# Performance work log

Measured on AMD Instinct MI355X. Metric: run time of the kernel, lower is better.

The kernel has to match this reference:

```python
import jax, jax.numpy as jnp
import numpy as np

EPS = 1e-5
SLOPE = 0.01  # nn.LeakyReLU default
K = 32
SIGMA = 1.0

def lrelu(x):
    return jnp.where(x >= 0, x, SLOPE * x)

def bn(x, gamma, beta, axes):
    # BatchNorm in training mode (fresh module, batch statistics)
    mu = jnp.mean(x, axis=axes, keepdims=True)
    var = jnp.var(x, axis=axes, keepdims=True)
    return (x - mu) * jax.lax.rsqrt(var + EPS) * gamma + beta

def knn_gather(x, k):
    # x: (B, N, C) -> neighbor features (B, N, k, C) by smallest squared distance
    sq = jnp.sum(x * x, axis=-1)
    d = sq[:, :, None] - 2.0 * jnp.einsum('bnc,bmc->bnm', x, x) + sq[:, None, :]
    idx = jax.lax.top_k(-d, k)[1]                      # (B, N, k)
    nbr = jax.vmap(lambda xb, ib: xb[ib])(x, idx)      # (B, N, k, C)
    return nbr

def edge_conv(x, w1, g1, b1, w2, g2, b2):
    # DGCNN EdgeConv: feat = [x_j - x_i, x_i] -> 1x1 conv/BN/LeakyReLU x2 -> max over k
    nbr = knn_gather(x, K)                             # (B, N, k, C)
    xc = x[:, :, None, :]
    feat = jnp.concatenate([nbr - xc, jnp.broadcast_to(xc, nbr.shape)], axis=-1)
    h = lrelu(bn(jnp.einsum('bnkc,oc->bnko', feat, w1), g1, b1, (0, 1, 2)))
    h = lrelu(bn(jnp.einsum('bnkc,oc->bnko', h, w2), g2, b2, (0, 1, 2)))
    return jnp.max(h, axis=2)                          # (B, N, C_out)

def gaussian_kernel_conv(xnei, centers):
    # xnei: (B, N, k, C), centers: (O, C) -> (B, N, O)
    d = (jnp.sum(xnei * xnei, -1)[..., None]
         - 2.0 * jnp.einsum('bnkc,oc->bnko', xnei, centers)
         + jnp.sum(centers * centers, -1))
    return jnp.sum(jnp.exp(-d / (2.0 * SIGMA ** 2)), axis=2)

def setup_inputs() -> dict:
    key = jax.random.key(0)
    ks = jax.random.split(key, 16)
    s = 0.05
    return {
        'x': jax.random.normal(ks[0], (2, 3, 64, 64), jnp.float32),
        'kc_centers': jax.random.normal(ks[1], (128, 3), jnp.float32),
        'e1_w1': jax.random.normal(ks[2], (64, 6), jnp.float32) * s,
        'e1_g1': jnp.ones((64,), jnp.float32), 'e1_b1': jnp.zeros((64,), jnp.float32),
        'e1_w2': jax.random.normal(ks[3], (64, 64), jnp.float32) * s,
        'e1_g2': jnp.ones((64,), jnp.float32), 'e1_b2': jnp.zeros((64,), jnp.float32),
        'e2_w1': jax.random.normal(ks[4], (128, 128), jnp.float32) * s,
        'e2_g1': jnp.ones((128,), jnp.float32), 'e2_b1': jnp.zeros((128,), jnp.float32),
        'e2_w2': jax.random.normal(ks[5], (128, 128), jnp.float32) * s,
        'e2_g2': jnp.ones((128,), jnp.float32), 'e2_b2': jnp.zeros((128,), jnp.float32),
        'w1': jax.random.normal(ks[6], (1024, 256), jnp.float32) * s,
        'g1': jnp.ones((1024,), jnp.float32), 'b1': jnp.zeros((1024,), jnp.float32),
        'w2': jax.random.normal(ks[7], (512, 1024), jnp.float32) * s,
        'g2': jnp.ones((512,), jnp.float32), 'b2': jnp.zeros((512,), jnp.float32),
        'w3': jax.random.normal(ks[8], (256, 512), jnp.float32) * s,
        'g3': jnp.ones((256,), jnp.float32), 'b3': jnp.zeros((256,), jnp.float32),
        'w4': jax.random.normal(ks[9], (9, 256), jnp.float32) * s,
    }

def reference(x, kc_centers, e1_w1, e1_g1, e1_b1, e1_w2, e1_g2, e1_b2,
              e2_w1, e2_g1, e2_b1, e2_w2, e2_g2, e2_b2,
              w1, g1, b1, w2, g2, b2, w3, g3, b3, w4):
    bs, f, c, n = x.shape
    # knn over the (B, c*n, 3) point cloud
    pts = x.reshape(bs, -1, c * n).transpose(0, 2, 1)
    xnei = knn_gather(pts, K)                               # (B, c*n, K, 3)
    kernels = gaussian_kernel_conv(xnei, kc_centers)        # (B, c*n, 128)
    # EdgeConv chain on reshape-view (matches torch reshape semantics exactly)
    xe = x.reshape(bs, c * n, -1)                           # (B, c*n, 3)
    xe = edge_conv(xe, e1_w1, e1_g1, e1_b1, e1_w2, e1_g2, e1_b2)   # (B, c*n, 64)
    xe = edge_conv(xe, e2_w1, e2_g1, e2_b1, e2_w2, e2_g2, e2_b2)   # (B, c*n, 128)
    h = jnp.concatenate([xe.reshape(bs, -1, c, n),
                         kernels.transpose(0, 2, 1).reshape(bs, -1, c, n)], axis=1)  # (B,256,c,n)
    def cbr(h, w, g, b):
        h = jnp.einsum('bchw,oc->bohw', h, w)               # 1x1 conv, no bias
        return lrelu(bn(h, g[None, :, None, None], b[None, :, None, None], (0, 2, 3)))
    h = cbr(h, w1, g1, b1)
    h = cbr(h, w2, g2, b2)
    h = cbr(h, w3, g3, b3)
    h = jnp.einsum('bchw,oc->bohw', h, w4)                  # (B, 9, c, n)
    h = jnp.max(jnp.max(h, axis=3), axis=2)                 # (B, 9)
    out = h + jnp.eye(3, dtype=h.dtype).reshape(1, 9)
    return out.reshape(bs, 3, 3)
```

## Files before the change

### kernel.cpp

```cpp
#include <hip/hip_runtime.h>
#include <hip/hip_fp16.h>
#include <math.h>

#define WN 4096
#define NP 8192
#define KK 32
#define EPSB 1e-5f

typedef __attribute__((ext_vector_type(8))) short s8v;
typedef __attribute__((ext_vector_type(4))) short s4v;
typedef __attribute__((ext_vector_type(4))) float f4v;

__device__ __forceinline__ float lrelu(float x){ return fmaxf(x, 0.01f*x); }
__device__ __forceinline__ float rlane(float v, int c){
  return __int_as_float(__builtin_amdgcn_readlane(__float_as_int(v), c));
}
__device__ __forceinline__ short f2bf(float f){
  unsigned u = __float_as_uint(f);
  u = (u + 0x7fffu + ((u>>16)&1u)) >> 16;
  return (short)u;
}
__device__ __forceinline__ float bf2f(short s){
  return __uint_as_float(((unsigned)(unsigned short)s) << 16);
}

__global__ void k_prep(const float* __restrict__ x, float* __restrict__ pts, float* __restrict__ xe0,
                       float* __restrict__ sqp, float* __restrict__ sqe,
                       float4* __restrict__ pts4, float4* __restrict__ xe04){
  int i = blockIdx.x*256 + threadIdx.x;
  if(i >= NP) return;
  int b = i>>12, p = i&4095;
  const float* xb = x + b*12288;
  float a0 = xb[p], a1 = xb[4096+p], a2 = xb[8192+p];
  pts[i*3+0]=a0; pts[i*3+1]=a1; pts[i*3+2]=a2;
  float sp = (a0*a0 + a1*a1) + a2*a2;
  sqp[i] = sp;
  pts4[i] = make_float4(a0,a1,a2,sp);
  float e0 = xb[p*3+0], e1 = xb[p*3+1], e2 = xb[p*3+2];
  xe0[i*3+0]=e0; xe0[i*3+1]=e1; xe0[i*3+2]=e2;
  float se = (e0*e0 + e1*e1) + e2*e2;
  sqe[i] = se;
  xe04[i] = make_float4(e0,e1,e2,se);
}

__device__ __forceinline__ void bitonic64(float& d, int& m, int l){
  #pragma unroll
  for(int k=2;k<=64;k<<=1){
    #pragma unroll
    for(int j=k>>1;j>0;j>>=1){
      float pd = __shfl_xor(d, j);
      int pm = __shfl_xor(m, j);
      bool pLess = (pd < d);
      bool dirUp = ((l & k) == 0);
      bool lower = ((l & j) == 0);
      bool take = dirUp ? (lower ? pLess : !pLess) : (lower ? !pLess : pLess);
      if(take){ d = pd; m = pm; }
    }
  }
}

__device__ __forceinline__ void kmerge(const float2* __restrict__ buf, int cnt, int l,
                                       float& lv, int& li){
  __builtin_amdgcn_wave_barrier();
  float md; int mi;
  if(l < 32){ md = lv; mi = li; }
  else{
    int i = l - 32;
    if(i < cnt){ float2 e = buf[i]; md = e.x; mi = __float_as_int(e.y); }
    else{ md = 3.4e38f; mi = 0x7fffffff; }
  }
  bitonic64(md, mi, l);
  if(l < 32){ lv = md; li = mi; }
}

__device__ __forceinline__ void topk_buf(float d, int m, int l, float2* __restrict__ buf,
                                         int& cnt, float& thr, float& lv, int& li){
  bool alive = d < thr;
  unsigned long long mask = __ballot(alive);
  while(mask){
    int nsurv = __popcll(mask);
    int space = 32 - cnt;
    int prefix = __popcll(mask & ((1ull<<l)-1ull));
    bool store = alive && (prefix < space);
    if(store) buf[cnt + prefix] = make_float2(d, __int_as_float(m));
    cnt += (nsurv < space) ? nsurv : space;
    alive = alive && !store;
    if(cnt == 32){
      kmerge(buf, 32, l, lv, li);
      cnt = 0;
      thr = rlane(lv, 31);
      alive = alive && (d < thr);
    }
    mask = __ballot(alive);
  }
}

__global__ __launch_bounds__(256) void k_knn3(const float4* __restrict__ pnt4, int* __restrict__ idx){
  __shared__ float2 bufs[4][32];
  int l = threadIdx.x&63;
  int wid = threadIdx.x>>6;
  int q = blockIdx.x*4 + wid;
  int b = q>>12, qr = q&4095;
  const float4* pb = pnt4 + ((size_t)b<<12);
  float2* buf = bufs[wid];
  float4 qv = pb[qr];
  float q0=qv.x, q1=qv.y, q2=qv.z, sqq=qv.w;
  float4 nc = pb[l + 64];
  float dd; int mm = l;
  {
    float4 c = pb[l];
    float dot = q0*c.x + q1*c.y + q2*c.z;
    dd = (sqq - 2.0f*dot) + c.w;
  }
  bitonic64(dd, mm, l);
  float lv = (l<32) ? dd : 3.4e38f;
  int li = (l<32) ? mm : 0x7fffffff;
  float thr = rlane(lv, 31);
  int cnt = 0;
  #pragma unroll 4
  for(int j=1;j<64;j++){
    float4 c = nc;
    nc = pb[l + (((j+1)&63)<<6)];
    float dot = q0*c.x + q1*c.y + q2*c.z;
    float d = (sqq - 2.0f*dot) + c.w;
    topk_buf(d, l + (j<<6), l, buf, cnt, thr, lv, li);
  }
  if(cnt) kmerge(buf, cnt, l, lv, li);
  if(l < 32) idx[(size_t)q*KK + l] = li;
}

__global__ __launch_bounds__(256) void k_knn_sel(const __half2* __restrict__ D, int* __restrict__ idx){
  __shared__ float2 bufs[4][32];
  int l = threadIdx.x&63;
  int wid = threadIdx.x>>6;
  int q = blockIdx.x*4 + wid;
  int b = q>>12, qr = q&4095;
  const __half2* row = D + ((size_t)b<<23) + ((size_t)qr<<11);
  float2* buf = bufs[wid];
  __half2 h0 = row[l];
  __half2 nh = row[l + 64];
  float2 f0 = __half22float2(h0);
  float dmin, dmax; int mmin, mmax;
  if(f0.x <= f0.y){ dmin=f0.x; mmin=2*l;   dmax=f0.y; mmax=2*l+1; }
  else            { dmin=f0.y; mmin=2*l+1; dmax=f0.x; mmax=2*l;   }
  bitonic64(dmin, mmin, l);
  float lv = (l<32) ? dmin : 3.4e38f;
  int li = (l<32) ? mmin : 0x7fffffff;
  float thr = rlane(lv, 31);
  int cnt = 0;
  topk_buf(dmax, mmax, l, buf, cnt, thr, lv, li);
  #pragma unroll 4
  for(int j=1;j<32;j++){
    __half2 h = nh;
    nh = row[l + (((j+1)&31)<<6)];
    float2 g = __half22float2(h);
    int base = 2*(l + (j<<6));
    topk_buf(g.x, base,   l, buf, cnt, thr, lv, li);
    topk_buf(g.y, base+1, l, buf, cnt, thr, lv, li);
  }
  if(cnt) kmerge(buf, cnt, l, lv, li);
  if(l < 32) idx[(size_t)q*KK + l] = li;
}

__global__ __launch_bounds__(128) void k_gauss(const float* __restrict__ pts, const float* __restrict__ sqp,
                                               const int* __restrict__ idxP, const float* __restrict__ cen,
                                               float* __restrict__ kout){
  __shared__ float nbx[KK], nby[KK], nbz[KK], nsq[KK];
  int p = blockIdx.x; int b = p>>12; int t = threadIdx.x;
  if(t < KK){
    int id = idxP[(size_t)p*KK + t] + (b<<12);
    nbx[t]=pts[id*3]; nby[t]=pts[id*3+1]; nbz[t]=pts[id*3+2];
    nsq[t]=sqp[id];
  }
  __syncthreads();
  float c0=cen[t*3], c1=cen[t*3+1], c2=cen[t*3+2];
  float sqc=(c0*c0+c1*c1)+c2*c2;
  float acc=0.f;
  #pragma unroll
  for(int k=0;k<KK;k++){
    float dot = nbx[k]*c0 + nby[k]*c1 + nbz[k]*c2;
    float d = (nsq[k] - 2.0f*dot) + sqc;
    acc += __expf(-0.5f*d);
  }
  kout[(size_t)((b<<7)+t)*4096 + (p&4095)] = acc;
}

__global__ void k_fin(const float* __restrict__ psum, const float* __restrict__ psq, int NW, int C, float Nn,
                      const float* __restrict__ g, const float* __restrict__ be,
                      float* __restrict__ sc, float* __restrict__ sh){
  int o = blockIdx.x, t = threadIdx.x;
  float s=0.f, q=0.f;
  for(int w=t; w<NW; w+=256){ s += psum[(size_t)w*C+o]; q += psq[(size_t)w*C+o]; }
  __shared__ float ls[256], lq[256];
  ls[t]=s; lq[t]=q; __syncthreads();
  for(int st=128; st; st>>=1){ if(t<st){ ls[t]+=ls[t+st]; lq[t]+=lq[t+st]; } __syncthreads(); }
  if(t==0){
    float mu = ls[0]/Nn;
    float var = lq[0]/Nn - mu*mu; if(var<0.f) var=0.f;
    float s1 = g[o]*rsqrtf(var + EPSB);
    sc[o]=s1; sh[o]=be[o]-mu*s1;
  }
}

__global__ __launch_bounds__(256) void k_ec1mom(const float* __restrict__ xe0, const int* __restrict__ idx1,
                                                float* __restrict__ pmom){
  int tid = blockIdx.x*256 + threadIdx.x;
  int l = threadIdx.x & 63;
  int wid = tid >> 6;
  float a[27];
  #pragma unroll
  for(int v=0;v<27;v++) a[v]=0.f;
  #pragma unroll
  for(int u=0;u<2;u++){
    int s = tid*2 + u;
    int p = s>>5;
    int bb = (p>>12)<<12;
    int id = bb + idx1[s];
    const float* nb = xe0 + (size_t)id*3;
    const float* xc = xe0 + (size_t)p*3;
    float f[6];
    f[0]=nb[0]-xc[0]; f[1]=nb[1]-xc[1]; f[2]=nb[2]-xc[2];
    f[3]=xc[0]; f[4]=xc[1]; f[5]=xc[2];
    int v=0;
    #pragma unroll
    for(int i=0;i<6;i++){
      #pragma unroll
      for(int j=i;j<6;j++){ a[v] = fmaf(f[i], f[j], a[v]); v++; }
    }
    #pragma unroll
    for(int i=0;i<6;i++) a[21+i] += f[i];
  }
  #pragma unroll
  for(int v=0;v<27;v++){
    float t = a[v];
    #pragma unroll
    for(int off=32; off; off>>=1) t += __shfl_xor(t, off);
    if(l==0) pmom[v*2048 + wid] = t;
  }
}

__global__ void k_msum(const float* __restrict__ pmom, float* __restrict__ mom){
  int v = blockIdx.x; int t = threadIdx.x;
  float s=0.f;
  for(int i=t;i<2048;i+=256) s += pmom[v*2048+i];
  __shared__ float ls[256];
  ls[t]=s; __syncthreads();
  for(int st=128; st; st>>=1){ if(t<st) ls[t]+=ls[t+st]; __syncthreads(); }
  if(t==0) mom[v]=ls[0];
}

__global__ void k_ec1bn(const float* __restrict__ mom, const float* __restrict__ w1,
                        const float* __restrict__ g, const float* __restrict__ be,
                        float* __restrict__ sc, float* __restrict__ sh){
  __shared__ float M[27];
  int t = threadIdx.x;
  if(t<27) M[t]=mom[t];
  __syncthreads();
  if(t<64){
    float w[6];
    #pragma unroll
    for(int c=0;c<6;c++) w[c]=w1[t*6+c];
    float qf=0.f, m1=0.f;
    int v=0;
    #pragma unroll
    for(int i=0;i<6;i++){
      #pragma unroll
      for(int j=i;j<6;j++){ qf += (i==j?1.f:2.f)*w[i]*w[j]*M[v]; v++; }
    }
    #pragma unroll
    for(int i=0;i<6;i++) m1 += w[i]*M[21+i];
    float N = 262144.f;
    float mu = m1/N;
    float var = qf/N - mu*mu; if(var<0.f) var=0.f;
    float s1 = g[t]*rsqrtf(var + EPSB);
    sc[t]=s1; sh[t]=be[t]-mu*s1;
  }
}

__global__ __launch_bounds__(256) void k_ec1g2m(const float* __restrict__ xe0, const int* __restrict__ idx1,
                                                const short* __restrict__ w2b, const float* __restrict__ w1,
                                                const float* __restrict__ s1, const float* __restrict__ t1,
                                                float* __restrict__ h2m, float* __restrict__ psum,
                                                float* __restrict__ psq){
  __shared__ short sA[8192], sB[8192];
  __shared__ float feat[6][128];
  __shared__ float w1l[384];
  __shared__ float bnS[64], bnT[64];
  __shared__ float srs[4][64], srq[4][64];
  int t = threadIdx.x;
  int blk = blockIdx.x;
  int s0 = blk*128;
  int pbase = s0>>5;
  int bb = (s0>>17)<<12;
  #pragma unroll
  for(int i=0;i<4;i++){
    int slot = t + i*256;
    *(s8v*)&sA[slot*8] = *(const s8v*)&w2b[slot*8];
  }
  for(int i=t; i<384; i+=256) w1l[i] = w1[i];
  if(t<64){ bnS[t]=s1[t]; bnT[t]=t1[t]; }
  if(t < 128){
    int s = s0 + t;
    int p = pbase + (t>>5);
    int id = bb + idx1[s];
    const float* nb = xe0 + (size_t)id*3;
    const float* xc = xe0 + (size_t)p*3;
    float x0 = xc[0], x1 = xc[1], x2 = xc[2];
    feat[0][t] = nb[0]-x0; feat[1][t] = nb[1]-x1; feat[2][t] = nb[2]-x2;
    feat[3][t] = x0; feat[4][t] = x1; feat[5][t] = x2;
  }
  __syncthreads();
  #pragma unroll
  for(int i=0;i<4;i++){
    int e = t + (i<<8);
    int n = e & 127;
    int kb8 = e >> 7;
    int k0 = kb8*8;
    float f0=feat[0][n], f1=feat[1][n], f2=feat[2][n];
    float f3=feat[3][n], f4=feat[4][n], f5=feat[5][n];
    s8v r;
    #pragma unroll
    for(int j=0;j<8;j++){
      int k = k0 + j;
      float h = w1l[k*6+0]*f0 + w1l[k*6+1]*f1 + w1l[k*6+2]*f2
              + w1l[k*6+3]*f3 + w1l[k*6+4]*f4 + w1l[k*6+5]*f5;
      r[j] = f2bf(lrelu(fmaf(h, bnS[k], bnT[k])));
    }
    int chunk = (k0>>5)*8 + (n>>4);
    int lane_ = ((k0>>3)&3)*16 + (n&15);
    *(s8v*)&sB[chunk*512 + lane_*8] = r;
  }
  __syncthreads();
  int lane = t&63, w = t>>6;
  f4v acc[4][2];
  #pragma unroll
  for(int i=0;i<4;i++){
    #pragma unroll
    for(int j=0;j<2;j++) acc[i][j] = (f4v)(0.f);
  }
  #pragma unroll
  for(int kh=0;kh<2;kh++){
    s8v av[4], bv[2];
    #pragma unroll
    for(int f=0;f<4;f++) av[f] = *(const s8v*)&sA[(kh*8 + f)*512 + lane*8];
    #pragma unroll
    for(int g=0;g<2;g++) bv[g] = *(const s8v*)&sB[(kh*8 + w*2 + g)*512 + lane*8];
    #pragma unroll
    for(int fm=0;fm<4;fm++){
      #pragma unroll
      for(int fn=0;fn<2;fn++)
        acc[fm][fn] = __builtin_amdgcn_mfma_f32_16x16x32_bf16(av[fm], bv[fn], acc[fm][fn], 0, 0, 0);
    }
  }
  int l15 = lane&15, l4 = (lane>>4)*4;
  int point = pbase + w;
  #pragma unroll
  for(int fm=0;fm<4;fm++){
    #pragma unroll
    for(int r=0;r<4;r++){
      int m = fm*16 + l4 + r;
      float a0 = acc[fm][0][r], a1 = acc[fm][1][r];
      float sr = a0 + a1;
      float sq = a0*a0 + a1*a1;
      float mx = fmaxf(a0, a1);
      #pragma unroll
      for(int off=1; off<16; off<<=1){
        sr += __shfl_xor(sr, off);
        sq += __shfl_xor(sq, off);
        mx = fmaxf(mx, __shfl_xor(mx, off));
      }
      if(l15==0){
        srs[w][m] = sr; srq[w][m] = sq;
        h2m[(size_t)point*64 + m] = mx;
      }
    }
  }
  __syncthreads();
  if(t<64){
    psum[(size_t)blk*64+t] = (srs[0][t]+srs[1][t]) + (srs[2][t]+srs[3][t]);
    psq[(size_t)blk*64+t]  = (srq[0][t]+srq[1][t]) + (srq[2][t]+srq[3][t]);
  }
}

__global__ __launch_bounds__(256) void k_ec1fin(const float* __restrict__ h2m, const float* __restrict__ s2,
                                                const float* __restrict__ t2, float* __restrict__ xe1,
                                                float* __restrict__ xe1T, float* __restrict__ sqx){
  int gid = blockIdx.x*256 + threadIdx.x;
  int p = gid>>6, l = gid&63;
  float v = lrelu(fmaf(h2m[(size_t)p*64+l], s2[l], t2[l]));
  xe1[(size_t)p*64+l] = v;
  int b=p>>12, pr=p&4095;
  xe1T[(size_t)(b*64+l)*4096 + pr] = v;
  float sq = v*v;
  #pragma unroll
  for(int off=32; off; off>>=1) sq += __shfl_xor(sq, off);
  if(l==0) sqx[p]=sq;
}

__global__ __launch_bounds__(256) void k_dgemm_m(const short* __restrict__ X, const float* __restrict__ sqx,
                                                 __half* __restrict__ D){
  __shared__ short sA[8192], sB[8192];
  int t = threadIdx.x;
  int lane = t&63, w = t>>6;
  int wm4 = (w>>1)*4, wn4 = (w&1)*4;
  int mb = blockIdx.y, nb = blockIdx.x, b = blockIdx.z;
  const short* AG = X + (size_t)(b*32 + mb)*8192;
  const short* BG = X + (size_t)(b*32 + nb)*8192;
  #pragma unroll
  for(int i=0;i<4;i++){
    int slot = t + i*256;
    *(s8v*)&sA[slot*8] = *(const s8v*)&AG[slot*8];
    *(s8v*)&sB[slot*8] = *(const s8v*)&BG[slot*8];
  }
  __syncthreads();
  f4v acc[4][4];
  #pragma unroll
  for(int i=0;i<4;i++){
    #pragma unroll
    for(int j=0;j<4;j++) acc[i][j] = (f4v)(0.f);
  }
  #pragma unroll
  for(int kh=0;kh<2;kh++){
    s8v av[4], bv[4];
    #pragma unroll
    for(int f=0;f<4;f++) av[f] = *(const s8v*)&sA[(kh*8 + wm4 + f)*512 + lane*8];
    #pragma unroll
    for(int f=0;f<4;f++) bv[f] = *(const s8v*)&sB[(kh*8 + wn4 + f)*512 + lane*8];
    #pragma unroll
    for(int fm=0;fm<4;fm++){
      #pragma unroll
      for(int fn=0;fn<4;fn++)
        acc[fm][fn] = __builtin_amdgcn_mfma_f32_16x16x32_bf16(av[fm], bv[fn], acc[fm][fn], 0, 0, 0);
    }
  }
  const float* sb = sqx + (b<<12);
  __half* Db = D + ((size_t)b<<24);
  int l15 = lane&15, l4 = (lane>>4)*4;
  #pragma unroll
  for(int fm=0;fm<4;fm++){
    int m0 = mb*128 + wm4*16 + fm*16 + l4;
    float sm0 = sb[m0], sm1 = sb[m0+1], sm2 = sb[m0+2], sm3 = sb[m0+3];
    #pragma unroll
    for(int fn=0;fn<4;fn++){
      int n = nb*128 + wn4*16 + fn*16 + l15;
      float sqn = sb[n];
      __half2 h01 = __floats2half2_rn((sm0 + sqn) - 2.f*acc[fm][fn][0],
                                      (sm1 + sqn) - 2.f*acc[fm][fn][1]);
      __half2 h23 = __floats2half2_rn((sm2 + sqn) - 2.f*acc[fm][fn][2],
                                      (sm3 + sqn) - 2.f*acc[fm][fn][3]);
      __half2* p = (__half2*)&Db[(size_t)n*4096 + m0];
      p[0] = h01; p[1] = h23;
    }
  }
}

__global__ __launch_bounds__(256) void k_ec2m1(const float* __restrict__ xe1, const int* __restrict__ idx2,
                                               const short* __restrict__ wb, short* __restrict__ h1,
                                               float* __restrict__ psum, float* __restrict__ psq){
  __shared__ short sA[8192], sB[8192];
  __shared__ float cts[4][64];
  __shared__ int nid[128];
  __shared__ float srs[2][128], srq[2][128];
  int t = threadIdx.x;
  int blk = blockIdx.x;
  int s0 = blk*128;
  int pbase = s0>>5;
  int bb = (s0>>17)<<12;
  if(t<128) nid[t] = (idx2[s0+t] + bb)<<6;
  cts[t>>6][t&63] = xe1[(size_t)(pbase + (t>>6))*64 + (t&63)];
  int lane = t&63, w = t>>6;
  int wm4 = (w>>1)*4, wn4 = (w&1)*4;
  f4v acc[4][4];
  #pragma unroll
  for(int i=0;i<4;i++){
    #pragma unroll
    for(int j=0;j<4;j++) acc[i][j] = (f4v)(0.f);
  }
  for(int st=0; st<2; ++st){
    __syncthreads();
    #pragma unroll
    for(int i=0;i<4;i++){
      int slot = t + i*256;
      *(s8v*)&sA[slot*8] = *(const s8v*)&wb[st*8192 + slot*8];
      int chunk = slot>>6, li = slot&63;
      int n = (chunk&7)*16 + (li&15);
      int c = ((chunk>>3)<<5) + ((li>>4)<<3);
      float v[8];
      if(st==0){
        const float* src = xe1 + nid[n] + c;
        float4 a0 = *(const float4*)src;
        float4 a1 = *(const float4*)(src+4);
        const float* cc = &cts[n>>5][c];
        float4 c0 = *(const float4*)cc;
        float4 c1 = *(const float4*)(cc+4);
        v[0]=a0.x-c0.x; v[1]=a0.y-c0.y; v[2]=a0.z-c0.z; v[3]=a0.w-c0.w;
        v[4]=a1.x-c1.x; v[5]=a1.y-c1.y; v[6]=a1.z-c1.z; v[7]=a1.w-c1.w;
      } else {
        const float* cc = &cts[n>>5][c];
        float4 c0 = *(const float4*)cc;
        float4 c1 = *(const float4*)(cc+4);
        v[0]=c0.x; v[1]=c0.y; v[2]=c0.z; v[3]=c0.w;
        v[4]=c1.x; v[5]=c1.y; v[6]=c1.z; v[7]=c1.w;
      }
      s8v r;
      #pragma unroll
      for(int j=0;j<8;j++) r[j] = f2bf(v[j]);
      *(s8v*)&sB[slot*8] = r;
    }
    __syncthreads();
    #pragma unroll
    for(int kh=0;kh<2;kh++){
      s8v av[4], bv[4];
      #pragma unroll
      for(int f=0;f<4;f++) av[f] = *(const s8v*)&sA[(kh*8 + wm4 + f)*512 + lane*8];
      #pragma unroll
      for(int f=0;f<4;f++) bv[f] = *(const s8v*)&sB[(kh*8 + wn4 + f)*512 + lane*8];
      #pragma unroll
      for(int fm=0;fm<4;fm++){
        #pragma unroll
        for(int fn=0;fn<4;fn++)
          acc[fm][fn] = __builtin_amdgcn_mfma_f32_16x16x32_bf16(av[fm], bv[fn], acc[fm][fn], 0, 0, 0);
      }
    }
  }
  int l15 = lane&15, l4 = (lane>>4)<<2;
  #pragma unroll
  for(int fm=0;fm<4;fm++){
    int mb_ = wm4*16 + fm*16 + l4;
    #pragma unroll
    for(int fn=0;fn<4;fn++){
      int n = wn4*16 + fn*16 + l15;
      s4v hw;
      hw[0]=f2bf(acc[fm][fn][0]); hw[1]=f2bf(acc[fm][fn][1]);
      hw[2]=f2bf(acc[fm][fn][2]); hw[3]=f2bf(acc[fm][fn][3]);
      *(s4v*)&h1[(size_t)(s0+n)*128 + mb_] = hw;
    }
    #pragma unroll
    for(int r=0;r<4;r++){
      float sr = (acc[fm][0][r]+acc[fm][1][r]) + (acc[fm][2][r]+acc[fm][3][r]);
      float sq = (acc[fm][0][r]*acc[fm][0][r]+acc[fm][1][r]*acc[fm][1][r])
               + (acc[fm][2][r]*acc[fm][2][r]+acc[fm][3][r]*acc[fm][3][r]);
      #pragma unroll
      for(int off=1; off<16; off<<=1){ sr += __shfl_xor(sr, off); sq += __shfl_xor(sq, off); }
      if(l15==0){ srs[w&1][mb_+r] = sr; srq[w&1][mb_+r] = sq; }
    }
  }
  __syncthreads();
  if(t<128){
    psum[(size_t)blk*128+t] = srs[0][t]+srs[1][t];
    psq[(size_t)blk*128+t]  = srq[0][t]+srq[1][t];
  }
}

__global__ __launch_bounds__(256) void k_ec2m2(const short* __restrict__ h1, const short* __restrict__ wb,
                                               const float* __restrict__ s1, const float* __restrict__ t1,
                                               float* __restrict__ h2max, float* __restrict__ psum,
                                               float* __restrict__ psq){
  __shared__ short sA[8192], sB[8192];
  __shared__ float bnS[128], bnT[128];
  __shared__ float srs[2][128], srq[2][128];
  int t = threadIdx.x;
  int blk = blockIdx.x;
  int s0 = blk*128;
  int pbase = s0>>5;
  if(t<128){ bnS[t]=s1[t]; bnT[t]=t1[t]; }
  int lane = t&63, w = t>>6;
  int wm4 = (w>>1)*4, wn4 = (w&1)*4;
  f4v acc[4][4];
  #pragma unroll
  for(int i=0;i<4;i++){
    #pragma unroll
    for(int j=0;j<4;j++) acc[i][j] = (f4v)(0.f);
  }
  for(int st=0; st<2; ++st){
    __syncthreads();
    #pragma unroll
    for(int i=0;i<4;i++){
      int slot = t + i*256;
      *(s8v*)&sA[slot*8] = *(const s8v*)&wb[st*8192 + slot*8];
      int chunk = slot>>6, li = slot&63;
      int n = (chunk&7)*16 + (li&15);
      int c = st*64 + ((chunk>>3)<<5) + ((li>>4)<<3);
      s8v hv = *(const s8v*)&h1[(size_t)(s0+n)*128 + c];
      s8v r;
      #pragma unroll
      for(int j=0;j<8;j++){
        float v = bf2f(hv[j]);
        r[j] = f2bf(lrelu(fmaf(v, bnS[c+j], bnT[c+j])));
      }
      *(s8v*)&sB[slot*8] = r;
    }
    __syncthreads();
    #pragma unroll
    for(int kh=0;kh<2;kh++){
      s8v av[4], bv[4];
      #pragma unroll
      for(int f=0;f<4;f++) av[f] = *(const s8v*)&sA[(kh*8 + wm4 + f)*512 + lane*8];
      #pragma unroll
      for(int f=0;f<4;f++) bv[f] = *(const s8v*)&sB[(kh*8 + wn4 + f)*512 + lane*8];
      #pragma unroll
      for(int fm=0;fm<4;fm++){
        #pragma unroll
        for(int fn=0;fn<4;fn++)
          acc[fm][fn] = __builtin_amdgcn_mfma_f32_16x16x32_bf16(av[fm], bv[fn], acc[fm][fn], 0, 0, 0);
      }
    }
  }
  int l15 = lane&15, l4 = (lane>>4)<<2;
  int pp0 = wn4>>1;
  #pragma unroll
  for(int fm=0;fm<4;fm++){
    int mb_ = wm4*16 + fm*16 + l4;
    #pragma unroll
    for(int r=0;r<4;r++){
      float sr = (acc[fm][0][r]+acc[fm][1][r]) + (acc[fm][2][r]+acc[fm][3][r]);
      float sq = (acc[fm][0][r]*acc[fm][0][r]+acc[fm][1][r]*acc[fm][1][r])
               + (acc[fm][2][r]*acc[fm][2][r]+acc[fm][3][r]*acc[fm][3][r]);
      float m0 = fmaxf(acc[fm][0][r], acc[fm][1][r]);
      float m1 = fmaxf(acc[fm][2][r], acc[fm][3][r]);
      #pragma unroll
      for(int off=1; off<16; off<<=1){ sr += __shfl_xor(sr, off); sq += __shfl_xor(sq, off); }
      #pragma unroll
      for(int off=1; off<16; off<<=1){ m0 = fmaxf(m0, __shfl_xor(m0, off)); m1 = fmaxf(m1, __shfl_xor(m1, off)); }
      if(l15==0){
        srs[w&1][mb_+r] = sr; srq[w&1][mb_+r] = sq;
        h2max[(size_t)(pbase+pp0)*128   + mb_+r] = m0;
        h2max[(size_t)(pbase+pp0+1)*128 + mb_+r] = m1;
      }
    }
  }
  __syncthreads();
  if(t<128){
    psum[(size_t)blk*128+t] = srs[0][t]+srs[1][t];
    psq[(size_t)blk*128+t]  = srq[0][t]+srq[1][t];
  }
}

__global__ void k_xe2fin(float* __restrict__ xe2, const float* __restrict__ s2, const float* __restrict__ t2){
  int i = blockIdx.x*256 + threadIdx.x;
  if(i >= NP*128) return;
  int o = i&127;
  xe2[i] = lrelu(fmaf(xe2[i], s2[o], t2[o]));
}

__global__ void k_transpose(const float* __restrict__ w, float* __restrict__ wT, int O, int C){
  int i = blockIdx.x*256 + threadIdx.x;
  if(i >= O*C) return;
  int o = i / C, c = i % C;
  wT[(size_t)c*O + o] = w[i];
}

__global__ void k_wprep(const float* __restrict__ w, short* __restrict__ wb, int M, int K){
  int tid = blockIdx.x*256 + threadIdx.x;
  int m = tid % M, kb8 = tid / M;
  int k0 = kb8*8;
  float4 v0 = *(const float4*)&w[(size_t)m*K + k0];
  float4 v1 = *(const float4*)&w[(size_t)m*K + k0 + 4];
  s8v r;
  r[0]=f2bf(v0.x); r[1]=f2bf(v0.y); r[2]=f2bf(v0.z); r[3]=f2bf(v0.w);
  r[4]=f2bf(v1.x); r[5]=f2bf(v1.y); r[6]=f2bf(v1.z); r[7]=f2bf(v1.w);
  int region = (m>>7)*(K>>6) + (k0>>6);
  int chunk = ((kb8>>2)&1)*8 + ((m>>4)&7);
  int lane = (kb8&3)*16 + (m&15);
  *(s8v*)&wb[(size_t)region*8192 + chunk*512 + lane*8] = r;
}

__global__ void k_bprep(const float* __restrict__ in, const float* __restrict__ sc, const float* __restrict__ sh,
                        short* __restrict__ ob, int K){
  int tid = blockIdx.x*256 + threadIdx.x;
  int n = tid & 8191, kb8 = tid >> 13;
  int k0 = kb8*8;
  int b = n>>12, s = n&4095;
  const float* ib = in + ((size_t)b*K + k0)*4096 + s;
  float v[8];
  #pragma unroll
  for(int j=0;j<8;j++) v[j] = ib[(size_t)j*4096];
  if(sc){
    #pragma unroll
    for(int j=0;j<8;j++) v[j] = lrelu(fmaf(v[j], sc[k0+j], sh[k0+j]));
  }
  s8v r;
  #pragma unroll
  for(int j=0;j<8;j++) r[j] = f2bf(v[j]);
  int region = (n>>7)*(K>>6) + (k0>>6);
  int chunk = ((kb8>>2)&1)*8 + ((n>>4)&7);
  int lane = (kb8&3)*16 + (n&15);
  *(s8v*)&ob[(size_t)region*8192 + chunk*512 + lane*8] = r;
}

__global__ void k_bprep1(const float* __restrict__ xe2, const float* __restrict__ kr,
                         short* __restrict__ ob){
  int tid = blockIdx.x*256 + threadIdx.x;
  int n = tid & 8191, kb8 = tid >> 13;
  int k0 = kb8*8;
  int b = n>>12, s = n&4095;
  const float* ib;
  if(k0 < 128) ib = xe2 + (size_t)b*524288 + (size_t)k0*4096 + s;
  else         ib = kr + ((size_t)(b*128 + (k0-128)))*4096 + s;
  float v[8];
  #pragma unroll
  for(int j=0;j<8;j++) v[j] = ib[(size_t)j*4096];
  s8v r;
  #pragma unroll
  for(int j=0;j<8;j++) r[j] = f2bf(v[j]);
  int region = (n>>7)*4 + (k0>>6);
  int chunk = ((kb8>>2)&1)*8 + ((n>>4)&7);
  int lane = (kb8&3)*16 + (n&15);
  *(s8v*)&ob[(size_t)region*8192 + chunk*512 + lane*8] = r;
}

__global__ __launch_bounds__(256) void k_gmm(const short* __restrict__ A, const short* __restrict__ B,
                                             float* __restrict__ out, int M, int K){
  __shared__ short sA[8192], sB[8192];
  int t = threadIdx.x;
  int lane = t&63;
  int w = t>>6;
  int wm4 = (w>>1)*4, wn4 = (w&1)*4;
  int mb = blockIdx.y, nb = blockIdx.x;
  int ksteps = K>>6;
  const short* AG = A + (size_t)mb*ksteps*8192;
  const short* BG = B + (size_t)nb*ksteps*8192;
  f4v acc[4][4];
  #pragma unroll
  for(int i=0;i<4;i++){
    #pragma unroll
    for(int j=0;j<4;j++) acc[i][j] = (f4v)(0.f);
  }
  for(int st=0; st<ksteps; ++st){
    __syncthreads();
    #pragma unroll
    for(int i=0;i<4;i++){
      int slot = t + i*256;
      *(s8v*)&sA[slot*8] = *(const s8v*)&AG[(size_t)st*8192 + slot*8];
      *(s8v*)&sB[slot*8] = *(const s8v*)&BG[(size_t)st*8192 + slot*8];
    }
    __syncthreads();
    #pragma unroll
    for(int kh=0;kh<2;kh++){
      s8v av[4], bv[4];
      #pragma unroll
      for(int f=0;f<4;f++) av[f] = *(const s8v*)&sA[(kh*8 + wm4 + f)*512 + lane*8];
      #pragma unroll
      for(int f=0;f<4;f++) bv[f] = *(const s8v*)&sB[(kh*8 + wn4 + f)*512 + lane*8];
      #pragma unroll
      for(int fm=0;fm<4;fm++){
        #pragma unroll
        for(int fn=0;fn<4;fn++)
          acc[fm][fn] = __builtin_amdgcn_mfma_f32_16x16x32_bf16(av[fm], bv[fn], acc[fm][fn], 0, 0, 0);
      }
    }
  }
  int l15 = lane&15, l4 = (lane>>4)*4;
  #pragma unroll
  for(int fm=0;fm<4;fm++){
    int mrow = mb*128 + wm4*16 + fm*16 + l4;
    #pragma unroll
    for(int fn=0;fn<4;fn++){
      int n = nb*128 + wn4*16 + fn*16 + l15;
      int b = n>>12, s = n&4095;
      float* ob = out + ((size_t)b*M + mrow)*4096 + s;
      #pragma unroll
      for(int r=0;r<4;r++) ob[(size_t)r*4096] = acc[fm][fn][r];
    }
  }
}

__global__ void k_cstats(const float* __restrict__ buf, int C, const float* __restrict__ g,
                         const float* __restrict__ be, float* __restrict__ sc, float* __restrict__ sh){
  int o = blockIdx.x, t = threadIdx.x;
  float s=0.f, q=0.f;
  for(int i=t;i<8192;i+=256){
    int b=i>>12, ss_=i&4095;
    float v = buf[(size_t)(b*C+o)*4096 + ss_];
    s+=v; q+=v*v;
  }
  __shared__ float ls[256], lq[256];
  ls[t]=s; lq[t]=q; __syncthreads();
  for(int st=128; st; st>>=1){ if(t<st){ ls[t]+=ls[t+st]; lq[t]+=lq[t+st]; } __syncthreads(); }
  if(t==0){
    float mu = ls[0]/8192.f;
    float var = lq[0]/8192.f - mu*mu; if(var<0.f) var=0.f;
    float s1 = g[o]*rsqrtf(var + EPSB);
    sc[o]=s1; sh[o]=be[o]-mu*s1;
  }
}

__global__ __launch_bounds__(256) void k_final4(const float* __restrict__ c3, const float* __restrict__ w4T,
                                                const float* __restrict__ sc, const float* __restrict__ sh,
                                                float* __restrict__ pmax){
  int b = blockIdx.y, st = blockIdx.x;
  int t = threadIdx.x; int s = st*256 + t;
  float acc[9];
  #pragma unroll
  for(int j=0;j<9;j++) acc[j]=0.f;
  const float* ib = c3 + (size_t)b*256*4096;
  for(int c=0;c<256;c++){
    float x = lrelu(fmaf(ib[(size_t)c*4096+s], sc[c], sh[c]));
    #pragma unroll
    for(int j=0;j<9;j++) acc[j]=fmaf(x, w4T[c*9+j], acc[j]);
  }
  __shared__ float red[256];
  for(int j=0;j<9;j++){
    red[t]=acc[j]; __syncthreads();
    for(int stp=128; stp; stp>>=1){ if(t<stp) red[t]=fmaxf(red[t],red[t+stp]); __syncthreads(); }
    if(t==0) pmax[(b*16+st)*9 + j]=red[0];
    __syncthreads();
  }
}

__global__ void k_out(const float* __restrict__ pmax, float* __restrict__ out){
  int i = threadIdx.x;
  if(i<18){
    int b=i/9, o=i%9;
    float m=-3.4e38f;
    for(int k=0;k<16;k++) m=fmaxf(m, pmax[(b*16+k)*9+o]);
    out[i] = m + ((o==0||o==4||o==8)?1.f:0.f);
  }
}

extern "C" void kernel_launch(void* const* d_in, const int* in_sizes, int n_in,
                              void* d_out, int out_size, void* d_ws, size_t ws_size,
                              hipStream_t stream){
  const float* x    = (const float*)d_in[0];
  const float* kc   = (const float*)d_in[1];
  const float* e1w1 = (const float*)d_in[2];
  const float* e1g1 = (const float*)d_in[3];
  const float* e1b1 = (const float*)d_in[4];
  const float* e1w2 = (const float*)d_in[5];
  const float* e1g2 = (const float*)d_in[6];
  const float* e1b2 = (const float*)d_in[7];
  const float* e2w1 = (const float*)d_in[8];
  const float* e2g1 = (const float*)d_in[9];
  const float* e2b1 = (const float*)d_in[10];
  const float* e2w2 = (const float*)d_in[11];
  const float* e2g2 = (const float*)d_in[12];
  const float* e2b2 = (const float*)d_in[13];
  const float* w1   = (const float*)d_in[14];
  const float* g1   = (const float*)d_in[15];
  const float* b1   = (const float*)d_in[16];
  const float* w2   = (const float*)d_in[17];
  const float* g2   = (const float*)d_in[18];
  const float* b2   = (const float*)d_in[19];
  const float* w3   = (const float*)d_in[20];
  const float* g3   = (const float*)d_in[21];
  const float* b3   = (const float*)d_in[22];
  const float* w4   = (const float*)d_in[23];

  if(ws_size < 156061696ull) return;
  char* ws = (char*)d_ws;
  float* pts   = (float*)(ws + 0);
  float* xe0   = (float*)(ws + 98304);
  float* sqp   = (float*)(ws + 196608);
  float* sqe   = (float*)(ws + 229376);
  float* sqx1  = (float*)(ws + 262144);
  float* xe1   = (float*)(ws + 294912);
  float* xe1T  = (float*)(ws + 2392064);
  float* xe2   = (float*)(ws + 4489216);
  float* kr    = (float*)(ws + 8683520);
  int*   idxP  = (int*)  (ws + 12877824);
  int*   idx1  = (int*)  (ws + 13926400);
  int*   idx2  = (int*)  (ws + 14974976);
  float* psum  = (float*)(ws + 16023552);
  float* psq   = (float*)(ws + 17072128);
  float* par   = (float*)(ws + 18120704);
  float* pmax  = (float*)(ws + 18153472);
  short* wb0   = (short*)(ws + 18157568);
  float* wT4   = (float*)(ws + 21827584);
  float* hbuf  = (float*)(ws + 21843968);
  short* wbe1  = (short*)(ws + 0);
  short* wbe2  = (short*)(ws + 65536);
  float4* pts4 = (float4*)(ws + 4489216);
  float4* xe04 = (float4*)(ws + 4489216 + 131072);
  short* actB  = (short*)(ws + 88952832);
  short* xpack = (short*)(ws + 88952832);
  short* h1b   = (short*)(ws + 21843968);
  short* wb1   = (short*)(ws + 105730048);
  short* wb2   = (short*)(ws + 106254336);
  short* wb3   = (short*)(ws + 107302912);
  float* pmom  = psum;
  float* momv  = psq;

  float* e1s1 = par+0;    float* e1t1 = par+64;
  float* e1s2 = par+128;  float* e1t2 = par+192;
  float* e2s1 = par+256;  float* e2t1 = par+384;
  float* e2s2 = par+512;  float* e2t2 = par+640;
  float* c1s  = par+768;  float* c1t  = par+1792;
  float* c2s  = par+2816; float* c2t  = par+3328;
  float* c3s  = par+3840; float* c3t  = par+4096;

  float* c1out = hbuf + 2097152;
  float* c2out = hbuf + 10485760;
  float* c3out = hbuf + 14680064;

  hipLaunchKernelGGL(k_prep, dim3(32), dim3(256), 0, stream, x, pts, xe0, sqp, sqe, pts4, xe04);
  hipLaunchKernelGGL(k_knn3, dim3(2048), dim3(256), 0, stream, pts4, idxP);
  hipLaunchKernelGGL(k_knn3, dim3(2048), dim3(256), 0, stream, xe04, idx1);
  hipLaunchKernelGGL(k_gauss, dim3(8192), dim3(128), 0, stream, pts, sqp, idxP, kc, kr);

  hipLaunchKernelGGL(k_wprep, dim3(2), dim3(256), 0, stream, e1w2, wb0, 64, 64);
  hipLaunchKernelGGL(k_ec1mom, dim3(512), dim3(256), 0, stream, xe0, idx1, pmom);
  hipLaunchKernelGGL(k_msum, dim3(27), dim3(256), 0, stream, pmom, momv);
  hipLaunchKernelGGL(k_ec1bn, dim3(1), dim3(64), 0, stream, momv, e1w1, e1g1, e1b1, e1s1, e1t1);
  hipLaunchKernelGGL(k_ec1g2m, dim3(2048), dim3(256), 0, stream, xe0, idx1, wb0, e1w1, e1s1, e1t1, hbuf, psum, psq);
  hipLaunchKernelGGL(k_fin, dim3(64), dim3(256), 0, stream, psum, psq, 2048, 64, 262144.f, e1g2, e1b2, e1s2, e1t2);
  hipLaunchKernelGGL(k_ec1fin, dim3(2048), dim3(256), 0, stream, hbuf, e1s2, e1t2, xe1, xe1T, sqx1);

  hipLaunchKernelGGL(k_wprep, dim3(256), dim3(256), 0, stream, xe1, xpack, 8192, 64);
  hipLaunchKernelGGL(k_dgemm_m, dim3(32,32,2), dim3(256), 0, stream, xpack, sqx1, (__half*)hbuf);
  hipLaunchKernelGGL(k_knn_sel, dim3(2048), dim3(256), 0, stream, (const __half2*)hbuf, idx2);

  hipLaunchKernelGGL(k_wprep, dim3(8), dim3(256), 0, stream, e2w1, wbe1, 128, 128);
  hipLaunchKernelGGL(k_wprep, dim3(8), dim3(256), 0, stream, e2w2, wbe2, 128, 128);
  hipLaunchKernelGGL(k_ec2m1, dim3(2048), dim3(256), 0, stream, xe1, idx2, wbe1, h1b, psum, psq);
  hipLaunchKernelGGL(k_fin, dim3(128), dim3(256), 0, stream, psum, psq, 2048, 128, 262144.f, e2g1, e2b1, e2s1, e2t1);
  hipLaunchKernelGGL(k_ec2m2, dim3(2048), dim3(256), 0, stream, h1b, wbe2, e2s1, e2t1, xe2, psum, psq);
  hipLaunchKernelGGL(k_fin, dim3(128), dim3(256), 0, stream, psum, psq, 2048, 128, 262144.f, e2g2, e2b2, e2s2, e2t2);
  hipLaunchKernelGGL(k_xe2fin, dim3(4096), dim3(256), 0, stream, xe2, e2s2, e2t2);

  hipLaunchKernelGGL(k_wprep, dim3(128), dim3(256), 0, stream, w1, wb1, 1024, 256);
  hipLaunchKernelGGL(k_wprep, dim3(256), dim3(256), 0, stream, w2, wb2, 512, 1024);
  hipLaunchKernelGGL(k_wprep, dim3(64),  dim3(256), 0, stream, w3, wb3, 256, 512);
  hipLaunchKernelGGL(k_transpose, dim3((9*256+255)/256), dim3(256), 0, stream, w4, wT4, 9, 256);

  hipLaunchKernelGGL(k_bprep1, dim3(1024), dim3(256), 0, stream, xe2, kr, actB);
  hipLaunchKernelGGL(k_gmm, dim3(64,8), dim3(256), 0, stream, wb1, actB, c1out, 1024, 256);
  hipLaunchKernelGGL(k_cstats, dim3(1024), dim3(256), 0, stream, c1out, 1024, g1, b1, c1s, c1t);

  hipLaunchKernelGGL(k_bprep, dim3(4096), dim3(256), 0, stream, c1out, c1s, c1t, actB, 1024);
  hipLaunchKernelGGL(k_gmm, dim3(64,4), dim3(256), 0, stream, wb2, actB, c2out, 512, 1024);
  hipLaunchKernelGGL(k_cstats, dim3(512), dim3(256), 0, stream, c2out, 512, g2, b2, c2s, c2t);

  hipLaunchKernelGGL(k_bprep, dim3(2048), dim3(256), 0, stream, c2out, c2s, c2t, actB, 512);
  hipLaunchKernelGGL(k_gmm, dim3(64,2), dim3(256), 0, stream, wb3, actB, c3out, 256, 512);
  hipLaunchKernelGGL(k_cstats, dim3(256), dim3(256), 0, stream, c3out, 256, g3, b3, c3s, c3t);

  hipLaunchKernelGGL(k_final4, dim3(16,2), dim3(256), 0, stream, c3out, wT4, c3s, c3t, pmax);
  hipLaunchKernelGGL(k_out, dim3(1), dim3(32), 0, stream, pmax, (float*)d_out);
}
```

Baseline: 517.2 us.

## Recompute first EdgeConv2 GEMM in fused kernel instead of storing h1 intermediate

```diff
diff --git a/kernel.cpp b/kernel.cpp
--- a/kernel.cpp
+++ b/kernel.cpp
@@ -454,9 +454,9 @@
   }
 }
 
-__global__ __launch_bounds__(256) void k_ec2m1(const float* __restrict__ xe1, const int* __restrict__ idx2,
-                                               const short* __restrict__ wb, short* __restrict__ h1,
-                                               float* __restrict__ psum, float* __restrict__ psq){
+__global__ __launch_bounds__(256) void k_ec2s(const float* __restrict__ xe1, const int* __restrict__ idx2,
+                                              const short* __restrict__ wb,
+                                              float* __restrict__ psum, float* __restrict__ psq){
   __shared__ short sA[8192], sB[8192];
   __shared__ float cts[4][64];
   __shared__ int nid[128];
@@ -528,14 +528,6 @@
   for(int fm=0;fm<4;fm++){
     int mb_ = wm4*16 + fm*16 + l4;
     #pragma unroll
-    for(int fn=0;fn<4;fn++){
-      int n = wn4*16 + fn*16 + l15;
-      s4v hw;
-      hw[0]=f2bf(acc[fm][fn][0]); hw[1]=f2bf(acc[fm][fn][1]);
-      hw[2]=f2bf(acc[fm][fn][2]); hw[3]=f2bf(acc[fm][fn][3]);
-      *(s4v*)&h1[(size_t)(s0+n)*128 + mb_] = hw;
-    }
-    #pragma unroll
     for(int r=0;r<4;r++){
       float sr = (acc[fm][0][r]+acc[fm][1][r]) + (acc[fm][2][r]+acc[fm][3][r]);
       float sq = (acc[fm][0][r]*acc[fm][0][r]+acc[fm][1][r]*acc[fm][1][r])
@@ -552,18 +544,24 @@
   }
 }
 
-__global__ __launch_bounds__(256) void k_ec2m2(const short* __restrict__ h1, const short* __restrict__ wb,
-                                               const float* __restrict__ s1, const float* __restrict__ t1,
-                                               float* __restrict__ h2max, float* __restrict__ psum,
-                                               float* __restrict__ psq){
+__global__ __launch_bounds__(256) void k_ec2f(const float* __restrict__ xe1, const int* __restrict__ idx2,
+                                              const short* __restrict__ wb1e, const short* __restrict__ wb2e,
+                                              const float* __restrict__ s1, const float* __restrict__ t1,
+                                              float* __restrict__ h2max, float* __restrict__ psum,
+                                              float* __restrict__ psq){
   __shared__ short sA[8192], sB[8192];
+  __shared__ short h1L[128*136];
+  __shared__ float cts[4][64];
+  __shared__ int nid[128];
   __shared__ float bnS[128], bnT[128];
   __shared__ float srs[2][128], srq[2][128];
   int t = threadIdx.x;
   int blk = blockIdx.x;
   int s0 = blk*128;
   int pbase = s0>>5;
-  if(t<128){ bnS[t]=s1[t]; bnT[t]=t1[t]; }
+  int bb = (s0>>17)<<12;
+  if(t<128){ nid[t] = (idx2[s0+t] + bb)<<6; bnS[t]=s1[t]; bnT[t]=t1[t]; }
+  cts[t>>6][t&63] = xe1[(size_t)(pbase + (t>>6))*64 + (t&63)];
   int lane = t&63, w = t>>6;
   int wm4 = (w>>1)*4, wn4 = (w&1)*4;
   f4v acc[4][4];
@@ -577,17 +575,30 @@
     #pragma unroll
     for(int i=0;i<4;i++){
       int slot = t + i*256;
-      *(s8v*)&sA[slot*8] = *(const s8v*)&wb[st*8192 + slot*8];
+      *(s8v*)&sA[slot*8] = *(const s8v*)&wb1e[st*8192 + slot*8];
       int chunk = slot>>6, li = slot&63;
       int n = (chunk&7)*16 + (li&15);
-      int c = st*64 + ((chunk>>3)<<5) + ((li>>4)<<3);
-      s8v hv = *(const s8v*)&h1[(size_t)(s0+n)*128 + c];
+      int c = ((chunk>>3)<<5) + ((li>>4)<<3);
+      float v[8];
+      if(st==0){
+        const float* src = xe1 + nid[n] + c;
+        float4 a0 = *(const float4*)src;
+        float4 a1 = *(const float4*)(src+4);
+        const float* cc = &cts[n>>5][c];
+        float4 c0 = *(const float4*)cc;
+        float4 c1 = *(const float4*)(cc+4);
+        v[0]=a0.x-c0.x; v[1]=a0.y-c0.y; v[2]=a0.z-c0.z; v[3]=a0.w-c0.w;
+        v[4]=a1.x-c1.x; v[5]=a1.y-c1.y; v[6]=a1.z-c1.z; v[7]=a1.w-c1.w;
+      } else {
+        const float* cc = &cts[n>>5][c];
+        float4 c0 = *(const float4*)cc;
+        float4 c1 = *(const float4*)(cc+4);
+        v[0]=c0.x; v[1]=c0.y; v[2]=c0.z; v[3]=c0.w;
+        v[4]=c1.x; v[5]=c1.y; v[6]=c1.z; v[7]=c1.w;
+      }
       s8v r;
       #pragma unroll
-      for(int j=0;j<8;j++){
-        float v = bf2f(hv[j]);
-        r[j] = f2bf(lrelu(fmaf(v, bnS[c+j], bnT[c+j])));
-      }
+      for(int j=0;j<8;j++) r[j] = f2bf(v[j]);
       *(s8v*)&sB[slot*8] = r;
     }
     __syncthreads();
@@ -607,17 +618,66 @@
     }
   }
   int l15 = lane&15, l4 = (lane>>4)<<2;
-  int pp0 = wn4>>1;
   #pragma unroll
   for(int fm=0;fm<4;fm++){
     int mb_ = wm4*16 + fm*16 + l4;
+    float b0 = bnS[mb_], b1 = bnS[mb_+1], b2 = bnS[mb_+2], b3 = bnS[mb_+3];
+    float c0 = bnT[mb_], c1 = bnT[mb_+1], c2 = bnT[mb_+2], c3 = bnT[mb_+3];
+    #pragma unroll
+    for(int fn=0;fn<4;fn++){
+      int n = wn4*16 + fn*16 + l15;
+      s4v hw;
+      hw[0]=f2bf(lrelu(fmaf(acc[fm][fn][0], b0, c0)));
+      hw[1]=f2bf(lrelu(fmaf(acc[fm][fn][1], b1, c1)));
+      hw[2]=f2bf(lrelu(fmaf(acc[fm][fn][2], b2, c2)));
+      hw[3]=f2bf(lrelu(fmaf(acc[fm][fn][3], b3, c3)));
+      *(s4v*)&h1L[n*136 + mb_] = hw;
+    }
+  }
+  f4v acc2[4][4];
+  #pragma unroll
+  for(int i=0;i<4;i++){
+    #pragma unroll
+    for(int j=0;j<4;j++) acc2[i][j] = (f4v)(0.f);
+  }
+  for(int st=0; st<2; ++st){
+    __syncthreads();
+    #pragma unroll
+    for(int i=0;i<4;i++){
+      int slot = t + i*256;
+      *(s8v*)&sA[slot*8] = *(const s8v*)&wb2e[st*8192 + slot*8];
+      int chunk = slot>>6, li = slot&63;
+      int n = (chunk&7)*16 + (li&15);
+      int c = st*64 + ((chunk>>3)<<5) + ((li>>4)<<3);
+      *(s8v*)&sB[slot*8] = *(const s8v*)&h1L[n*136 + c];
+    }
+    __syncthreads();
+    #pragma unroll
+    for(int kh=0;kh<2;kh++){
+      s8v av[4], bv[4];
+      #pragma unroll
+      for(int f=0;f<4;f++) av[f] = *(const s8v*)&sA[(kh*8 + wm4 + f)*512 + lane*8];
+      #pragma unroll
+      for(int f=0;f<4;f++) bv[f] = *(const s8v*)&sB[(kh*8 + wn4 + f)*512 + lane*8];
+      #pragma unroll
+      for(int fm=0;fm<4;fm++){
+        #pragma unroll
+        for(int fn=0;fn<4;fn++)
+          acc2[fm][fn] = __builtin_amdgcn_mfma_f32_16x16x32_bf16(av[fm], bv[fn], acc2[fm][fn], 0, 0, 0);
+      }
+    }
+  }
+  int pp0 = wn4>>1;
+  #pragma unroll
+  for(int fm=0;fm<4;fm++){
+    int mb_ = wm4*16 + fm*16 + l4;
     #pragma unroll
     for(int r=0;r<4;r++){
-      float sr = (acc[fm][0][r]+acc[fm][1][r]) + (acc[fm][2][r]+acc[fm][3][r]);
-      float sq = (acc[fm][0][r]*acc[fm][0][r]+acc[fm][1][r]*acc[fm][1][r])
-               + (acc[fm][2][r]*acc[fm][2][r]+acc[fm][3][r]*acc[fm][3][r]);
-      float m0 = fmaxf(acc[fm][0][r], acc[fm][1][r]);
-      float m1 = fmaxf(acc[fm][2][r], acc[fm][3][r]);
+      float sr = (acc2[fm][0][r]+acc2[fm][1][r]) + (acc2[fm][2][r]+acc2[fm][3][r]);
+      float sq = (acc2[fm][0][r]*acc2[fm][0][r]+acc2[fm][1][r]*acc2[fm][1][r])
+               + (acc2[fm][2][r]*acc2[fm][2][r]+acc2[fm][3][r]*acc2[fm][3][r]);
+      float m0 = fmaxf(acc2[fm][0][r], acc2[fm][1][r]);
+      float m1 = fmaxf(acc2[fm][2][r], acc2[fm][3][r]);
       #pragma unroll
       for(int off=1; off<16; off<<=1){ sr += __shfl_xor(sr, off); sq += __shfl_xor(sq, off); }
       #pragma unroll
@@ -873,7 +933,6 @@
   float4* xe04 = (float4*)(ws + 4489216 + 131072);
   short* actB  = (short*)(ws + 88952832);
   short* xpack = (short*)(ws + 88952832);
-  short* h1b   = (short*)(ws + 21843968);
   short* wb1   = (short*)(ws + 105730048);
   short* wb2   = (short*)(ws + 106254336);
   short* wb3   = (short*)(ws + 107302912);
@@ -911,9 +970,9 @@
 
   hipLaunchKernelGGL(k_wprep, dim3(8), dim3(256), 0, stream, e2w1, wbe1, 128, 128);
   hipLaunchKernelGGL(k_wprep, dim3(8), dim3(256), 0, stream, e2w2, wbe2, 128, 128);
-  hipLaunchKernelGGL(k_ec2m1, dim3(2048), dim3(256), 0, stream, xe1, idx2, wbe1, h1b, psum, psq);
+  hipLaunchKernelGGL(k_ec2s, dim3(2048), dim3(256), 0, stream, xe1, idx2, wbe1, psum, psq);
   hipLaunchKernelGGL(k_fin, dim3(128), dim3(256), 0, stream, psum, psq, 2048, 128, 262144.f, e2g1, e2b1, e2s1, e2t1);
-  hipLaunchKernelGGL(k_ec2m2, dim3(2048), dim3(256), 0, stream, h1b, wbe2, e2s1, e2t1, xe2, psum, psq);
+  hipLaunchKernelGGL(k_ec2f, dim3(2048), dim3(256), 0, stream, xe1, idx2, wbe1, wbe2, e2s1, e2t1, xe2, psum, psq);
   hipLaunchKernelGGL(k_fin, dim3(128), dim3(256), 0, stream, psum, psq, 2048, 128, 262144.f, e2g2, e2b2, e2s2, e2t2);
   hipLaunchKernelGGL(k_xe2fin, dim3(4096), dim3(256), 0, stream, xe2, e2s2, e2t2);
 
```

Result: slower. 527.7 us (+2.0%).
